# Kernel optimization log

Measured on AMD Instinct MI355X. Metric: run time of the kernel, lower is better.

Reference implementation:

```python
import jax, jax.numpy as jnp
import numpy as np

# 6 ordered (src, tgt) pairs among 3 modalities, in the same nested-loop order as torch
SRC = jnp.array([0, 0, 1, 1, 2, 2])
TGT = jnp.array([1, 2, 0, 2, 0, 1])

B, L, H, G = 16384, 256, 96, 32
P = 6  # number of translation directions


def _layernorm(x, gamma, beta, eps=1e-5):
    # x: [P, B, F]; gamma/beta: [P, 1, F]
    m = jnp.mean(x, axis=-1, keepdims=True)
    v = jnp.mean((x - m) ** 2, axis=-1, keepdims=True)
    return (x - m) * jax.lax.rsqrt(v + eps) * gamma + beta


def setup_inputs() -> dict:
    key = jax.random.key(0)
    ks = jax.random.split(key, 20)
    f32 = jnp.float32
    d = {}
    d['mus'] = jax.random.normal(ks[0], (3, B, L), f32)
    d['logvars'] = jax.random.normal(ks[1], (3, B, L), f32)
    d['mask'] = jax.random.randint(ks[2], (B, 3), 0, 2).astype(bool)
    # translation head params (stacked over the 6 pairs)
    d['hw1'] = jax.random.normal(ks[3], (P, 2 * L, H), f32) / np.sqrt(2 * L)
    d['hb1'] = jax.random.normal(ks[4], (P, H), f32) * 0.02
    d['hg1'] = jnp.ones((P, H), f32)
    d['hbe1'] = jnp.zeros((P, H), f32)
    d['hw2'] = jax.random.normal(ks[5], (P, H, H), f32) / np.sqrt(H)
    d['hb2'] = jax.random.normal(ks[6], (P, H), f32) * 0.02
    d['hg2'] = jnp.ones((P, H), f32)
    d['hbe2'] = jnp.zeros((P, H), f32)
    d['hw3'] = jax.random.normal(ks[7], (P, H, 2 * L), f32) / np.sqrt(H)
    d['hb3'] = jax.random.normal(ks[8], (P, 2 * L), f32) * 0.02
    # gate network params
    d['gw1'] = jax.random.normal(ks[9], (P, 2 * L, G), f32) / np.sqrt(2 * L)
    d['gb1'] = jax.random.normal(ks[10], (P, G), f32) * 0.02
    d['gg1'] = jnp.ones((P, G), f32)
    d['gbe1'] = jnp.zeros((P, G), f32)
    d['gw2'] = jax.random.normal(ks[11], (P, G, 1), f32) / np.sqrt(G)
    d['gb2'] = jnp.full((P, 1), -1.0, f32)
    return d


def reference(mus, logvars, mask, hw1, hb1, hg1, hbe1, hw2, hb2, hg2, hbe2,
              hw3, hb3, gw1, gb1, gg1, gbe1, gw2, gb2):
    latent = mus.shape[-1]
    # gather source posteriors per pair and concat: [P, B, 2L]
    h = jnp.concatenate([mus[SRC], logvars[SRC]], axis=-1)
    # translation head: Linear -> LN -> GELU (x2) -> Linear
    x = jax.nn.gelu(_layernorm(jnp.einsum('pbi,pih->pbh', h, hw1) + hb1[:, None, :],
                               hg1[:, None, :], hbe1[:, None, :]), approximate=False)
    x = jax.nn.gelu(_layernorm(jnp.einsum('pbh,phk->pbk', x, hw2) + hb2[:, None, :],
                               hg2[:, None, :], hbe2[:, None, :]), approximate=False)
    out = jnp.einsum('pbh,pho->pbo', x, hw3) + hb3[:, None, :]  # [P, B, 2L]
    mu_pseudo = out[..., :latent]
    lv_pseudo = jnp.clip(out[..., latent:], -6.0, 2.0)
    # gate: Linear -> LN -> GELU -> Linear -> sigmoid
    g = jax.nn.gelu(_layernorm(jnp.einsum('pbi,pig->pbg', h, gw1) + gb1[:, None, :],
                               gg1[:, None, :], gbe1[:, None, :]), approximate=False)
    gate = jax.nn.sigmoid(jnp.einsum('pbg,pgo->pbo', g, gw2) + gb2[:, None, :])  # [P, B, 1]
    # only keep rows where source observed and target missing; others are zero-filled
    needs = (mask[:, SRC] & ~mask[:, TGT]).T  # [P, B]
    m3 = needs[:, :, None]
    zero = jnp.zeros((), mu_pseudo.dtype)
    return (jnp.where(m3, mu_pseudo, zero),
            jnp.where(m3, lv_pseudo, zero),
            jnp.where(m3, gate, zero))
```

## Files before the change

### kernel.cpp

```cpp
#include <hip/hip_runtime.h>
#include <hip/hip_bf16.h>
#include <math.h>

#define B_ 16384
#define NP 6

typedef short v8s __attribute__((ext_vector_type(8)));
typedef short v4s __attribute__((ext_vector_type(4)));
typedef float v4f __attribute__((ext_vector_type(4)));

__device__ __forceinline__ float gelu_f(float x) {
    return 0.5f * x * (1.0f + erff(x * 0.7071067811865476f));
}
__device__ __forceinline__ unsigned short f2bf(float f) {
    union { float f; unsigned u; } x; x.f = f;
    unsigned r = x.u + 0x7FFFu + ((x.u >> 16) & 1u);
    return (unsigned short)(r >> 16);
}
__device__ __forceinline__ short bfs(float f) {
    union { __hip_bfloat16 h; unsigned short u; } cv;
    cv.h = __float2bfloat16(f);
    return (short)cv.u;
}

__global__ __launch_bounds__(256) void k_pre(
    const int* __restrict__ mask, int* __restrict__ counts,
    int* __restrict__ lists, unsigned long long* __restrict__ nb,
    const float* __restrict__ hw1, const float* __restrict__ gw1,
    const float* __restrict__ hw2, const float* __restrict__ hw3,
    unsigned short* __restrict__ w1t, unsigned short* __restrict__ w2f,
    unsigned short* __restrict__ w3f)
{
    int t = threadIdx.x;
    if (blockIdx.x < 48) {
        int p   = blockIdx.x >> 3;
        int seg = blockIdx.x & 7;
        int src = p >> 1;
        int tgt = (0x102021 >> (p * 4)) & 0xF;
        int lane = t & 63;
        for (int it = 0; it < 8; ++it) {
            int b = seg * 2048 + it * 256 + t;
            int needs = (mask[b * 3 + src] != 0) && (mask[b * 3 + tgt] == 0);
            unsigned long long bal = __ballot(needs);
            int total = __popcll(bal);
            int base = 0;
            if (lane == 0) {
                nb[p * 256 + (b >> 6)] = bal;
                if (total) base = atomicAdd(&counts[p], total);
            }
            base = __shfl(base, 0, 64);
            if (needs) {
                int prefix = __popcll(bal & ((1ull << lane) - 1ull));
                lists[p * B_ + base + prefix] = b;
            }
        }
        return;
    }
    const int T1 = NP * 65536, T2 = NP * 9216, T3 = NP * 49152;
    for (int i = (blockIdx.x - 48) * 256 + t; i < T1 + T2 + T3; i += 512 * 256) {
        if (i < T1) {
            int p = i >> 16, rem = i & 65535, c = rem >> 9, k = rem & 511;
            float v = (c < 96) ? hw1[p * 49152 + k * 96 + c] : gw1[p * 16384 + k * 32 + (c - 96)];
            w1t[i] = f2bf(v);
        } else if (i < T1 + T2) {
            int j2 = i - T1, p = j2 / 9216, rem = j2 % 9216;
            int f = rem >> 9, within = rem & 511;
            int qg = within >> 3, j = within & 7;
            int q = qg >> 2, g = qg & 3;
            int k = (f % 3) * 32 + g * 8 + j;
            int col = (f / 3) * 16 + q;
            w2f[j2] = f2bf(hw2[p * 9216 + k * 96 + col]);
        } else {
            int j3 = i - T1 - T2, p = j3 / 49152, rem = j3 % 49152;
            int f = rem >> 9, within = rem & 511;
            int qg = within >> 3, j = within & 7;
            int q = qg >> 2, g = qg & 3;
            int k = (f % 3) * 32 + g * 8 + j;
            int col = (f / 3) * 16 + q;
            w3f[j3] = f2bf(hw3[p * 49152 + k * 512 + col]);
        }
    }
}

__global__ __launch_bounds__(512, 2) void k_main(
    const float* __restrict__ mus, const float* __restrict__ logvars,
    const unsigned short* __restrict__ w1t, const unsigned short* __restrict__ w2f,
    const unsigned short* __restrict__ w3f,
    const float* __restrict__ hb1, const float* __restrict__ hg1, const float* __restrict__ hbe1,
    const float* __restrict__ hb2, const float* __restrict__ hg2, const float* __restrict__ hbe2,
    const float* __restrict__ hb3,
    const float* __restrict__ gb1, const float* __restrict__ gg1, const float* __restrict__ gbe1,
    const float* __restrict__ gw2, const float* __restrict__ gb2,
    const int* __restrict__ counts, const int* __restrict__ lists,
    const unsigned long long* __restrict__ nb,
    float* __restrict__ out0, float* __restrict__ out1, float* __restrict__ out2)
{
    int cb = blockIdx.x;
    int p  = cb % 6, blk = cb / 6;
    int t  = threadIdx.x;
    int w  = t >> 6, l = t & 63, g = l >> 4, q = l & 15;
    int cnt = counts[p];

    __shared__ __align__(16) unsigned short smW[128 * 512];
    __shared__ __align__(16) unsigned short smX[8 * 1664];

    int chunk = (p < 4) ? 384 : 392;
    int pwr   = chunk >> 3;
    int zr0   = blk * chunk + w * pwr;
    int zend  = min(blk * chunk + chunk, B_);
    int zn    = max(0, min(zr0 + pwr, zend) - zr0);
    unsigned long long zw0 = 0ull, zw1 = 0ull;
    int wi0 = zr0 >> 6;
    if (zn > 0) {
        zw0 = nb[p * 256 + wi0];
        zw1 = nb[p * 256 + ((zr0 + zn - 1) >> 6)];
    }
    auto zburst = [&](int i0, int i1) {
        i1 = min(i1, zn);
        float4 z = make_float4(0.f, 0.f, 0.f, 0.f);
        for (int i = i0; i < i1; ++i) {
            int zr = zr0 + i;
            unsigned long long wd = ((zr >> 6) == wi0) ? zw0 : zw1;
            if (!((wd >> (zr & 63)) & 1ull)) {
                size_t rb = ((size_t)p * B_ + zr) * 256 + l * 4;
                *(float4*)(out0 + rb) = z;
                *(float4*)(out1 + rb) = z;
                if (l == 0) out2[p * B_ + zr] = 0.f;
            }
        }
    };

    bool anyStage = (blk * 128) < cnt;
    int start = (blk * 8 + w) * 16;
    bool active = start < cnt;
    int nr = active ? min(16, cnt - start) : 0;
    int myrow = active ? lists[p * B_ + min(start + q, cnt - 1)] : 0;
    const float* Ab = mus     + (size_t)(p >> 1) * B_ * 256 + (size_t)myrow * 256 + g * 8;
    const float* Lb = logvars + (size_t)(p >> 1) * B_ * 256 + (size_t)myrow * 256 + g * 8;

    const unsigned short* w1p = w1t + (size_t)p * 65536;
    const unsigned short* w2p = w2f + (size_t)p * 9216;
    const unsigned short* w3p = w3f + (size_t)p * 49152;

    float4 ma[8], mb[8];
    if (active) {
#pragma unroll
        for (int k = 0; k < 8; ++k) {
            ma[k] = *(const float4*)(Ab + k * 32);
            mb[k] = *(const float4*)(Ab + k * 32 + 4);
        }
    }
    zburst(0, 12);

    if (anyStage) {
        {
            int c = t >> 2, qt = t & 3;
            const unsigned short* src = w1p + c * 512 + qt * 128;
            unsigned short* dstrow = smW + c * 512;
            int cx = c & 7;
#pragma unroll
            for (int jj = 0; jj < 16; ++jj) {
                int j = qt * 16 + jj;
                *(v8s*)(dstrow + (((j ^ cx)) << 3)) = *(const v8s*)(src + jj * 8);
            }
        }
        __syncthreads();
    }

    unsigned short* mX = smX + w * 1664;
    float gb2p = gb2[p];

    if (active) {
        v4f acc1[8];
#pragma unroll
        for (int n = 0; n < 8; ++n) acc1[n] = (v4f){0.f, 0.f, 0.f, 0.f};

        int qx = q & 7;
        float4 la[8], lb[8];
#pragma unroll
        for (int kt = 0; kt < 8; ++kt) {
            la[kt] = *(const float4*)(Lb + kt * 32);
            lb[kt] = *(const float4*)(Lb + kt * 32 + 4);
            v8s a;
            a[0] = bfs(ma[kt].x); a[1] = bfs(ma[kt].y); a[2] = bfs(ma[kt].z); a[3] = bfs(ma[kt].w);
            a[4] = bfs(mb[kt].x); a[5] = bfs(mb[kt].y); a[6] = bfs(mb[kt].z); a[7] = bfs(mb[kt].w);
#pragma unroll
            for (int n = 0; n < 8; ++n) {
                int i = kt * 4 + g;
                v8s b = *(const v8s*)(smW + (n * 16 + q) * 512 + ((i ^ qx) << 3));
                acc1[n] = __builtin_amdgcn_mfma_f32_16x16x32_bf16(b, a, acc1[n], 0, 0, 0);
            }
        }
        zburst(12, 24);
#pragma unroll
        for (int kt = 0; kt < 8; ++kt) {
            v8s a;
            a[0] = bfs(la[kt].x); a[1] = bfs(la[kt].y); a[2] = bfs(la[kt].z); a[3] = bfs(la[kt].w);
            a[4] = bfs(lb[kt].x); a[5] = bfs(lb[kt].y); a[6] = bfs(lb[kt].z); a[7] = bfs(lb[kt].w);
#pragma unroll
            for (int n = 0; n < 8; ++n) {
                int i = (kt + 8) * 4 + g;
                v8s b = *(const v8s*)(smW + (n * 16 + q) * 512 + ((i ^ qx) << 3));
                acc1[n] = __builtin_amdgcn_mfma_f32_16x16x32_bf16(b, a, acc1[n], 0, 0, 0);
            }
        }

        {
            float vb[8][4];
#pragma unroll
            for (int n = 0; n < 8; ++n) {
                float4 bb = (n < 6) ? *(const float4*)(hb1 + p * 96 + n * 16 + 4 * g)
                                    : *(const float4*)(gb1 + p * 32 + (n - 6) * 16 + 4 * g);
                vb[n][0] = acc1[n][0] + bb.x; vb[n][1] = acc1[n][1] + bb.y;
                vb[n][2] = acc1[n][2] + bb.z; vb[n][3] = acc1[n][3] + bb.w;
            }
            float hs = 0.f;
#pragma unroll
            for (int n = 0; n < 6; ++n)
#pragma unroll
                for (int j = 0; j < 4; ++j) hs += vb[n][j];
            hs += __shfl_xor(hs, 16, 64); hs += __shfl_xor(hs, 32, 64);
            float mean = hs * (1.f / 96.f);
            float sq = 0.f;
#pragma unroll
            for (int n = 0; n < 6; ++n)
#pragma unroll
                for (int j = 0; j < 4; ++j) { float d = vb[n][j] - mean; sq += d * d; }
            sq += __shfl_xor(sq, 16, 64); sq += __shfl_xor(sq, 32, 64);
            float rs = rsqrtf(sq * (1.f / 96.f) + 1e-5f);
#pragma unroll
            for (int n = 0; n < 6; ++n) {
                float4 ga = *(const float4*)(hg1  + p * 96 + n * 16 + 4 * g);
                float4 be = *(const float4*)(hbe1 + p * 96 + n * 16 + 4 * g);
                v4s xo;
                xo[0] = bfs(gelu_f((vb[n][0] - mean) * rs * ga.x + be.x));
                xo[1] = bfs(gelu_f((vb[n][1] - mean) * rs * ga.y + be.y));
                xo[2] = bfs(gelu_f((vb[n][2] - mean) * rs * ga.z + be.z));
                xo[3] = bfs(gelu_f((vb[n][3] - mean) * rs * ga.w + be.w));
                *(v4s*)(mX + q * 104 + n * 16 + 4 * g) = xo;
            }
            float gs = 0.f;
#pragma unroll
            for (int n = 6; n < 8; ++n)
#pragma unroll
                for (int j = 0; j < 4; ++j) gs += vb[n][j];
            gs += __shfl_xor(gs, 16, 64); gs += __shfl_xor(gs, 32, 64);
            float mg = gs * (1.f / 32.f);
            float gq = 0.f;
#pragma unroll
            for (int n = 6; n < 8; ++n)
#pragma unroll
                for (int j = 0; j < 4; ++j) { float d = vb[n][j] - mg; gq += d * d; }
            gq += __shfl_xor(gq, 16, 64); gq += __shfl_xor(gq, 32, 64);
            float rg = rsqrtf(gq * (1.f / 32.f) + 1e-5f);
            float gv = 0.f;
#pragma unroll
            for (int n = 6; n < 8; ++n) {
                int cg = (n - 6) * 16 + 4 * g;
                float4 ga = *(const float4*)(gg1  + p * 32 + cg);
                float4 be = *(const float4*)(gbe1 + p * 32 + cg);
                float4 w2 = *(const float4*)(gw2  + p * 32 + cg);
                gv += gelu_f((vb[n][0] - mg) * rg * ga.x + be.x) * w2.x;
                gv += gelu_f((vb[n][1] - mg) * rg * ga.y + be.y) * w2.y;
                gv += gelu_f((vb[n][2] - mg) * rg * ga.z + be.z) * w2.z;
                gv += gelu_f((vb[n][3] - mg) * rg * ga.w + be.w) * w2.w;
            }
            gv += __shfl_xor(gv, 16, 64); gv += __shfl_xor(gv, 32, 64);
            if (g == 0 && q < nr)
                out2[p * B_ + myrow] = 1.f / (1.f + expf(-(gv + gb2p)));
        }

        {
            v4f acc2[6];
#pragma unroll
            for (int n = 0; n < 6; ++n) acc2[n] = (v4f){0.f, 0.f, 0.f, 0.f};
            int fo = q * 32 + g * 8;
#pragma unroll
            for (int kit = 0; kit < 3; ++kit) {
                v8s xa = *(const v8s*)(mX + q * 104 + kit * 32 + g * 8);
#pragma unroll
                for (int n = 0; n < 6; ++n) {
                    v8s wb = *(const v8s*)(w2p + (n * 3 + kit) * 512 + fo);
                    acc2[n] = __builtin_amdgcn_mfma_f32_16x16x32_bf16(wb, xa, acc2[n], 0, 0, 0);
                }
            }
            float vc[6][4];
#pragma unroll
            for (int n = 0; n < 6; ++n) {
                float4 bb = *(const float4*)(hb2 + p * 96 + n * 16 + 4 * g);
                vc[n][0] = acc2[n][0] + bb.x; vc[n][1] = acc2[n][1] + bb.y;
                vc[n][2] = acc2[n][2] + bb.z; vc[n][3] = acc2[n][3] + bb.w;
            }
            float hs = 0.f;
#pragma unroll
            for (int n = 0; n < 6; ++n)
#pragma unroll
                for (int j = 0; j < 4; ++j) hs += vc[n][j];
            hs += __shfl_xor(hs, 16, 64); hs += __shfl_xor(hs, 32, 64);
            float mean = hs * (1.f / 96.f);
            float sq = 0.f;
#pragma unroll
            for (int n = 0; n < 6; ++n)
#pragma unroll
                for (int j = 0; j < 4; ++j) { float d = vc[n][j] - mean; sq += d * d; }
            sq += __shfl_xor(sq, 16, 64); sq += __shfl_xor(sq, 32, 64);
            float rs = rsqrtf(sq * (1.f / 96.f) + 1e-5f);
#pragma unroll
            for (int n = 0; n < 6; ++n) {
                float4 ga = *(const float4*)(hg2  + p * 96 + n * 16 + 4 * g);
                float4 be = *(const float4*)(hbe2 + p * 96 + n * 16 + 4 * g);
                v4s xo;
                xo[0] = bfs(gelu_f((vc[n][0] - mean) * rs * ga.x + be.x));
                xo[1] = bfs(gelu_f((vc[n][1] - mean) * rs * ga.y + be.y));
                xo[2] = bfs(gelu_f((vc[n][2] - mean) * rs * ga.z + be.z));
                xo[3] = bfs(gelu_f((vc[n][3] - mean) * rs * ga.w + be.w));
                *(v4s*)(mX + q * 104 + n * 16 + 4 * g) = xo;
            }
        }
        zburst(24, 36);

        {
            size_t base = ((size_t)(p * B_ + myrow)) * 256;
            int fo = q * 32 + g * 8;
#pragma unroll 1
            for (int pc = 0; pc < 4; ++pc) {
                v4f acc3[8];
#pragma unroll
                for (int n = 0; n < 8; ++n) acc3[n] = (v4f){0.f, 0.f, 0.f, 0.f};
#pragma unroll
                for (int kit = 0; kit < 3; ++kit) {
                    v8s xa = *(const v8s*)(mX + q * 104 + kit * 32 + g * 8);
#pragma unroll
                    for (int n = 0; n < 8; ++n) {
                        v8s wb = *(const v8s*)(w3p + ((pc * 8 + n) * 3 + kit) * 512 + fo);
                        acc3[n] = __builtin_amdgcn_mfma_f32_16x16x32_bf16(wb, xa, acc3[n], 0, 0, 0);
                    }
                }
#pragma unroll
                for (int n = 0; n < 8; ++n) {
                    int c = pc * 128 + n * 16 + 4 * g;
                    float4 bb = *(const float4*)(hb3 + p * 512 + c);
                    if (q < nr) {
                        float o0 = acc3[n][0] + bb.x, o1 = acc3[n][1] + bb.y;
                        float o2 = acc3[n][2] + bb.z, o3 = acc3[n][3] + bb.w;
                        if (pc < 2) {
                            *(float4*)(out0 + base + c) = make_float4(o0, o1, o2, o3);
                        } else {
                            o0 = fminf(fmaxf(o0, -6.f), 2.f); o1 = fminf(fmaxf(o1, -6.f), 2.f);
                            o2 = fminf(fmaxf(o2, -6.f), 2.f); o3 = fminf(fmaxf(o3, -6.f), 2.f);
                            *(float4*)(out1 + base + c - 256) = make_float4(o0, o1, o2, o3);
                        }
                    }
                }
            }
        }
        zburst(36, pwr);
    } else {
        zburst(12, pwr);
    }
}

extern "C" void kernel_launch(void* const* d_in, const int* in_sizes, int n_in,
                              void* d_out, int out_size, void* d_ws, size_t ws_size,
                              hipStream_t stream)
{
    (void)in_sizes; (void)n_in; (void)out_size; (void)ws_size;

    const float* mus     = (const float*)d_in[0];
    const float* logvars = (const float*)d_in[1];
    const int*   mask    = (const int*)d_in[2];
    const float* hw1  = (const float*)d_in[3];
    const float* hb1  = (const float*)d_in[4];
    const float* hg1  = (const float*)d_in[5];
    const float* hbe1 = (const float*)d_in[6];
    const float* hw2  = (const float*)d_in[7];
    const float* hb2  = (const float*)d_in[8];
    const float* hg2  = (const float*)d_in[9];
    const float* hbe2 = (const float*)d_in[10];
    const float* hw3  = (const float*)d_in[11];
    const float* hb3  = (const float*)d_in[12];
    const float* gw1  = (const float*)d_in[13];
    const float* gb1  = (const float*)d_in[14];
    const float* gg1  = (const float*)d_in[15];
    const float* gbe1 = (const float*)d_in[16];
    const float* gw2  = (const float*)d_in[17];
    const float* gb2  = (const float*)d_in[18];

    float* out0 = (float*)d_out;
    float* out1 = out0 + (size_t)NP * B_ * 256;
    float* out2 = out1 + (size_t)NP * B_ * 256;

    int* counts = (int*)d_ws;
    int* lists  = counts + 16;
    unsigned short* w1t = (unsigned short*)(lists + NP * B_);
    unsigned short* w2f = w1t + (size_t)NP * 65536;
    unsigned short* w3f = w2f + (size_t)NP * 9216;
    unsigned long long* nbm = (unsigned long long*)(w3f + (size_t)NP * 49152);

    hipMemsetAsync(d_ws, 0, 64, stream);
    k_pre<<<dim3(560), dim3(256), 0, stream>>>(
        mask, counts, lists, nbm, hw1, gw1, hw2, hw3, w1t, w2f, w3f);
    k_main<<<dim3(256), dim3(512), 0, stream>>>(
        mus, logvars, w1t, w2f, w3f,
        hb1, hg1, hbe1, hb2, hg2, hbe2, hb3,
        gb1, gg1, gbe1, gw2, gb2,
        counts, lists, nbm, out0, out1, out2);
}
```

Baseline: 92.22 us.

## Drop LDS staging of first-layer weights; read fragment-ordered W1 from global

Rewrites the W1 preprocessing so the concatenated head/gate first-layer weights are stored in MFMA fragment order, letting each wave load its B operands straight from global/L2 instead of staging a 128KB transposed copy in shared memory behind a barrier. Workgroups shrink from 512 to 256 threads and the grid grows to 172 blocks per pair, with zero-fill bursts resized to match. With the large LDS buffer gone, more waves can be resident per CU. Explicit waitcnt barriers are added around the shared-memory handoff. The cost is repeated global loads of the same weights by every wave, which depend on cache hits.

```diff
diff --git a/kernel.cpp b/kernel.cpp
--- a/kernel.cpp
+++ b/kernel.cpp
@@ -4,6 +4,8 @@
 
 #define B_ 16384
 #define NP 6
+#define BLKP 172
+#define GRID (NP * BLKP)
 
 typedef short v8s __attribute__((ext_vector_type(8)));
 typedef short v4s __attribute__((ext_vector_type(4)));
@@ -28,7 +30,7 @@
     int* __restrict__ lists, unsigned long long* __restrict__ nb,
     const float* __restrict__ hw1, const float* __restrict__ gw1,
     const float* __restrict__ hw2, const float* __restrict__ hw3,
-    unsigned short* __restrict__ w1t, unsigned short* __restrict__ w2f,
+    unsigned short* __restrict__ w1f, unsigned short* __restrict__ w2f,
     unsigned short* __restrict__ w3f)
 {
     int t = threadIdx.x;
@@ -59,9 +61,15 @@
     const int T1 = NP * 65536, T2 = NP * 9216, T3 = NP * 49152;
     for (int i = (blockIdx.x - 48) * 256 + t; i < T1 + T2 + T3; i += 512 * 256) {
         if (i < T1) {
-            int p = i >> 16, rem = i & 65535, c = rem >> 9, k = rem & 511;
-            float v = (c < 96) ? hw1[p * 49152 + k * 96 + c] : gw1[p * 16384 + k * 32 + (c - 96)];
-            w1t[i] = f2bf(v);
+            int p = i >> 16, rem = i & 65535;
+            int f = rem >> 9, within = rem & 511;
+            int qg = within >> 3, j = within & 7;
+            int q = qg >> 2, g = qg & 3;
+            int kt = f >> 3, n = f & 7;
+            int k = kt * 32 + g * 8 + j;
+            int col = n * 16 + q;
+            float v = (col < 96) ? hw1[p * 49152 + k * 96 + col] : gw1[p * 16384 + k * 32 + (col - 96)];
+            w1f[i] = f2bf(v);
         } else if (i < T1 + T2) {
             int j2 = i - T1, p = j2 / 9216, rem = j2 % 9216;
             int f = rem >> 9, within = rem & 511;
@@ -82,9 +90,9 @@
     }
 }
 
-__global__ __launch_bounds__(512, 2) void k_main(
+__global__ __launch_bounds__(256) void k_main(
     const float* __restrict__ mus, const float* __restrict__ logvars,
-    const unsigned short* __restrict__ w1t, const unsigned short* __restrict__ w2f,
+    const unsigned short* __restrict__ w1f, const unsigned short* __restrict__ w2f,
     const unsigned short* __restrict__ w3f,
     const float* __restrict__ hb1, const float* __restrict__ hg1, const float* __restrict__ hbe1,
     const float* __restrict__ hb2, const float* __restrict__ hg2, const float* __restrict__ hbe2,
@@ -101,16 +109,12 @@
     int w  = t >> 6, l = t & 63, g = l >> 4, q = l & 15;
     int cnt = counts[p];
 
-    __shared__ __align__(16) unsigned short smW[128 * 512];
-    __shared__ __align__(16) unsigned short smX[8 * 1664];
-
-    int chunk = (p < 4) ? 384 : 392;
-    int pwr   = chunk >> 3;
-    int zr0   = blk * chunk + w * pwr;
-    int zend  = min(blk * chunk + chunk, B_);
-    int zn    = max(0, min(zr0 + pwr, zend) - zr0);
+    __shared__ __align__(16) unsigned short smX[4 * 1664];
+
+    int zr0  = blk * 96 + w * 24;
+    int zn   = max(0, min(zr0 + 24, B_) - zr0);
+    int wi0  = zr0 >> 6;
     unsigned long long zw0 = 0ull, zw1 = 0ull;
-    int wi0 = zr0 >> 6;
     if (zn > 0) {
         zw0 = nb[p * 256 + wi0];
         zw1 = nb[p * 256 + ((zr0 + zn - 1) >> 6)];
@@ -130,17 +134,19 @@
         }
     };
 
-    bool anyStage = (blk * 128) < cnt;
-    int start = (blk * 8 + w) * 16;
+    int start = (blk * 4 + w) * 16;
     bool active = start < cnt;
     int nr = active ? min(16, cnt - start) : 0;
     int myrow = active ? lists[p * B_ + min(start + q, cnt - 1)] : 0;
     const float* Ab = mus     + (size_t)(p >> 1) * B_ * 256 + (size_t)myrow * 256 + g * 8;
     const float* Lb = logvars + (size_t)(p >> 1) * B_ * 256 + (size_t)myrow * 256 + g * 8;
 
-    const unsigned short* w1p = w1t + (size_t)p * 65536;
+    const unsigned short* w1p = w1f + (size_t)p * 65536;
     const unsigned short* w2p = w2f + (size_t)p * 9216;
     const unsigned short* w3p = w3f + (size_t)p * 49152;
+    unsigned short* mX = smX + w * 1664;
+    float gb2p = gb2[p];
+    int fo = q * 32 + g * 8;
 
     float4 ma[8], mb[8];
     if (active) {
@@ -150,32 +156,13 @@
             mb[k] = *(const float4*)(Ab + k * 32 + 4);
         }
     }
-    zburst(0, 12);
-
-    if (anyStage) {
-        {
-            int c = t >> 2, qt = t & 3;
-            const unsigned short* src = w1p + c * 512 + qt * 128;
-            unsigned short* dstrow = smW + c * 512;
-            int cx = c & 7;
-#pragma unroll
-            for (int jj = 0; jj < 16; ++jj) {
-                int j = qt * 16 + jj;
-                *(v8s*)(dstrow + (((j ^ cx)) << 3)) = *(const v8s*)(src + jj * 8);
-            }
-        }
-        __syncthreads();
-    }
-
-    unsigned short* mX = smX + w * 1664;
-    float gb2p = gb2[p];
+    zburst(0, 6);
 
     if (active) {
         v4f acc1[8];
 #pragma unroll
         for (int n = 0; n < 8; ++n) acc1[n] = (v4f){0.f, 0.f, 0.f, 0.f};
 
-        int qx = q & 7;
         float4 la[8], lb[8];
 #pragma unroll
         for (int kt = 0; kt < 8; ++kt) {
@@ -186,12 +173,11 @@
             a[4] = bfs(mb[kt].x); a[5] = bfs(mb[kt].y); a[6] = bfs(mb[kt].z); a[7] = bfs(mb[kt].w);
 #pragma unroll
             for (int n = 0; n < 8; ++n) {
-                int i = kt * 4 + g;
-                v8s b = *(const v8s*)(smW + (n * 16 + q) * 512 + ((i ^ qx) << 3));
+                v8s b = *(const v8s*)(w1p + (kt * 8 + n) * 512 + fo);
                 acc1[n] = __builtin_amdgcn_mfma_f32_16x16x32_bf16(b, a, acc1[n], 0, 0, 0);
             }
         }
-        zburst(12, 24);
+        zburst(6, 12);
 #pragma unroll
         for (int kt = 0; kt < 8; ++kt) {
             v8s a;
@@ -199,8 +185,7 @@
             a[4] = bfs(lb[kt].x); a[5] = bfs(lb[kt].y); a[6] = bfs(lb[kt].z); a[7] = bfs(lb[kt].w);
 #pragma unroll
             for (int n = 0; n < 8; ++n) {
-                int i = (kt + 8) * 4 + g;
-                v8s b = *(const v8s*)(smW + (n * 16 + q) * 512 + ((i ^ qx) << 3));
+                v8s b = *(const v8s*)(w1p + ((kt + 8) * 8 + n) * 512 + fo);
                 acc1[n] = __builtin_amdgcn_mfma_f32_16x16x32_bf16(b, a, acc1[n], 0, 0, 0);
             }
         }
@@ -269,12 +254,12 @@
             if (g == 0 && q < nr)
                 out2[p * B_ + myrow] = 1.f / (1.f + expf(-(gv + gb2p)));
         }
+        __builtin_amdgcn_s_waitcnt(0);
 
         {
             v4f acc2[6];
 #pragma unroll
             for (int n = 0; n < 6; ++n) acc2[n] = (v4f){0.f, 0.f, 0.f, 0.f};
-            int fo = q * 32 + g * 8;
 #pragma unroll
             for (int kit = 0; kit < 3; ++kit) {
                 v8s xa = *(const v8s*)(mX + q * 104 + kit * 32 + g * 8);
@@ -317,11 +302,11 @@
                 *(v4s*)(mX + q * 104 + n * 16 + 4 * g) = xo;
             }
         }
-        zburst(24, 36);
+        __builtin_amdgcn_s_waitcnt(0);
+        zburst(12, 18);
 
         {
             size_t base = ((size_t)(p * B_ + myrow)) * 256;
-            int fo = q * 32 + g * 8;
 #pragma unroll 1
             for (int pc = 0; pc < 4; ++pc) {
                 v4f acc3[8];
@@ -354,9 +339,9 @@
                 }
             }
         }
-        zburst(36, pwr);
+        zburst(18, 24);
     } else {
-        zburst(12, pwr);
+        zburst(6, 24);
     }
 }
 
@@ -392,16 +377,16 @@
 
     int* counts = (int*)d_ws;
     int* lists  = counts + 16;
-    unsigned short* w1t = (unsigned short*)(lists + NP * B_);
-    unsigned short* w2f = w1t + (size_t)NP * 65536;
+    unsigned short* w1f = (unsigned short*)(lists + NP * B_);
+    unsigned short* w2f = w1f + (size_t)NP * 65536;
     unsigned short* w3f = w2f + (size_t)NP * 9216;
     unsigned long long* nbm = (unsigned long long*)(w3f + (size_t)NP * 49152);
 
     hipMemsetAsync(d_ws, 0, 64, stream);
     k_pre<<<dim3(560), dim3(256), 0, stream>>>(
-        mask, counts, lists, nbm, hw1, gw1, hw2, hw3, w1t, w2f, w3f);
-    k_main<<<dim3(256), dim3(512), 0, stream>>>(
-        mus, logvars, w1t, w2f, w3f,
+        mask, counts, lists, nbm, hw1, gw1, hw2, hw3, w1f, w2f, w3f);
+    k_main<<<dim3(GRID), dim3(256), 0, stream>>>(
+        mus, logvars, w1f, w2f, w3f,
         hb1, hg1, hbe1, hb2, hg2, hbe2, hb3,
         gb1, gg1, gbe1, gw2, gb2,
         counts, lists, nbm, out0, out1, out2);
```

New measurement: 99.02 us. 7.4% more time.
